# Kernel tuning notes

Measured on AMD Instinct MI355X. Metric: run time of the kernel, lower is better.

## Reference

```python
import jax, jax.numpy as jnp
import numpy as np

N_NODES = 40000

def setup_inputs() -> dict:
    key = jax.random.key(0)
    k1, k2, k3, k4 = jax.random.split(key, 4)
    x = jax.random.normal(k1, (N_NODES, 256), dtype=jnp.float32)
    edge_index = jax.random.randint(k2, (2, 640000), 0, N_NODES, dtype=jnp.int64)
    W = jax.random.normal(k3, (256, 128), dtype=jnp.float32) * (1.0 / np.sqrt(256))
    b = jax.random.normal(k4, (128,), dtype=jnp.float32) * 0.01
    return {"x": x, "edge_index": edge_index, "W": W, "b": b}

def reference(x, edge_index, W, b):
    N = x.shape[0]
    # GCNConv: add self-loops, symmetric degree normalization, linear, aggregate, bias
    loops = jnp.arange(N, dtype=edge_index.dtype)
    src = jnp.concatenate([edge_index[0], loops])  # message sources j
    dst = jnp.concatenate([edge_index[1], loops])  # targets i
    ones = jnp.ones_like(dst, dtype=x.dtype)
    deg = jax.ops.segment_sum(ones, dst, num_segments=N)  # in-degree incl. self-loop
    dinv = jnp.where(deg > 0, jax.lax.rsqrt(deg), 0.0)
    norm = dinv[src] * dinv[dst]  # [E+N]
    xw = x @ W  # transform first (in_dim -> out_dim), as in PyG GCNConv
    msgs = norm[:, None] * xw[src]  # [E+N, out_dim]
    agg = jax.ops.segment_sum(msgs, dst, num_segments=N) + b
    return jax.nn.relu(agg)  # dropout_value == 0 -> no dropout
```

## Files before the change

### kernel.cpp

```cpp
#include <hip/hip_runtime.h>

#define N_NODES 40000
#define IN_DIM 256
#define OUT_DIM 128
#define CAP 64
#define GEMM_BLOCKS 625
#define FILL_SLICES 160
#define FILL_RANGES 8
#define FILL_BLOCKS (FILL_SLICES * FILL_RANGES)
#define RANGE_SZ ((N_NODES + FILL_RANGES - 1) / FILL_RANGES)

typedef __bf16 bf16x8 __attribute__((ext_vector_type(8)));
typedef float floatx4 __attribute__((ext_vector_type(4)));

__device__ __forceinline__ int clamp_idx(int v) {
    unsigned u = (unsigned)v;
    return (u < (unsigned)N_NODES) ? v : 0;
}

__device__ __forceinline__ int get_idx(const void* p, long long i, int is64) {
    if (is64) return clamp_idx((int)((const long long*)p)[i]);
    return clamp_idx(((const int*)p)[i]);
}

__device__ __forceinline__ float bflo(unsigned u) {
    union { unsigned i; float f; } c; c.i = u << 16; return c.f;
}
__device__ __forceinline__ float bfhi(unsigned u) {
    union { unsigned i; float f; } c; c.i = u & 0xFFFF0000u; return c.f;
}

__global__ void prep_r13(const int* __restrict__ edge32, int* __restrict__ flag,
                         int* __restrict__ cnt, const float* __restrict__ W,
                         __bf16* __restrict__ wswz) {
    int i = blockIdx.x * 256 + threadIdx.x;
    if (i < N_NODES) cnt[i] = 0;
    if (i < IN_DIM * OUT_DIM) {
        int j    = i & 7;
        int lane = (i >> 3) & 63;
        int tile = i >> 9;
        int ct = tile & 7, kc = tile >> 3;
        int k = kc * 32 + (lane >> 4) * 8 + j;
        int n = ct * 16 + (lane & 15);
        wswz[i] = (__bf16)W[k * OUT_DIM + n];
    }
    if (blockIdx.x == 0) {
        __shared__ int sh[256];
        int t = threadIdx.x;
        int nz = 0;
        for (int k = t; k < 1000; k += 256) nz |= (edge32[2 * k + 1] != 0);
        sh[t] = nz;
        __syncthreads();
        for (int off = 128; off > 0; off >>= 1) {
            if (t < off) sh[t] |= sh[t + off];
            __syncthreads();
        }
        if (t == 0) *flag = sh[0] ? 0 : 1;
    }
}

__global__ __launch_bounds__(256) void main_r13(
    const float* __restrict__ x, const __bf16* __restrict__ wswz,
    __bf16* __restrict__ xwb,
    const void* __restrict__ edge, int E, const int* __restrict__ flag,
    int* __restrict__ cnt, unsigned short* __restrict__ bucket) {
    int t = threadIdx.x;
    if (blockIdx.x < GEMM_BLOCKS) {
        int wave = t >> 6, lane = t & 63;
        int quad = lane >> 4, m16 = lane & 15;
        int m = blockIdx.x * 64 + wave * 16 + m16;
        const float* xrow = x + (long long)m * IN_DIM;
        const bf16x8* wp = (const bf16x8*)wswz;

        floatx4 acc[8];
#pragma unroll
        for (int ct = 0; ct < 8; ++ct) acc[ct] = (floatx4){0.f, 0.f, 0.f, 0.f};

#pragma unroll
        for (int kc = 0; kc < 8; ++kc) {
            int k0 = kc * 32 + quad * 8;
            float4 xa = *(const float4*)(xrow + k0);
            float4 xb = *(const float4*)(xrow + k0 + 4);
            bf16x8 af;
            af[0] = (__bf16)xa.x; af[1] = (__bf16)xa.y;
            af[2] = (__bf16)xa.z; af[3] = (__bf16)xa.w;
            af[4] = (__bf16)xb.x; af[5] = (__bf16)xb.y;
            af[6] = (__bf16)xb.z; af[7] = (__bf16)xb.w;
#pragma unroll
            for (int ct = 0; ct < 8; ++ct) {
                bf16x8 bf = wp[(kc * 8 + ct) * 64 + lane];
                acc[ct] = __builtin_amdgcn_mfma_f32_16x16x32_bf16(af, bf, acc[ct], 0, 0, 0);
            }
        }

        int rbase = blockIdx.x * 64 + wave * 16 + quad * 4;
#pragma unroll
        for (int ct = 0; ct < 8; ++ct) {
            int col = ct * 16 + m16;
#pragma unroll
            for (int r = 0; r < 4; ++r)
                xwb[(long long)(rbase + r) * OUT_DIM + col] = (__bf16)acc[ct][r];
        }
    } else {
        int is64 = *flag;
        int fb = blockIdx.x - GEMM_BLOCKS;
        int range = blockIdx.x & 7;
        int slice = fb >> 3;
        int lo = range * RANGE_SZ;
        int slice_len = (E + FILL_SLICES - 1) / FILL_SLICES;
        int e0 = slice * slice_len;
        int e1 = e0 + slice_len; if (e1 > E) e1 = E;
        for (int e = e0 + t; e < e1; e += 256) {
            int d = get_idx(edge, (long long)E + e, is64);
            if ((unsigned)(d - lo) < (unsigned)RANGE_SZ) {
                int s = get_idx(edge, e, is64);
                int pos = atomicAdd(&cnt[d], 1);
                if (pos < CAP) bucket[d * CAP + pos] = (unsigned short)s;
            }
        }
    }
}

__global__ void gather_r13(const unsigned short* __restrict__ bucket,
                           const int* __restrict__ cnt,
                           const unsigned* __restrict__ xwd, const float* __restrict__ b,
                           float* __restrict__ out) {
    int node = blockIdx.x * 4 + (threadIdx.x >> 6);
    int lane = threadIdx.x & 63;
    if (node >= N_NODES) return;
    float b0 = b[2 * lane], b1 = b[2 * lane + 1];
    int cn_true = cnt[node];
    int take = cn_true < CAP ? cn_true : CAP;
    float dd = rsqrtf((float)(cn_true + 1));
    unsigned us = xwd[node * 64 + lane];
    float a0 = dd * dd * bflo(us);
    float a1 = dd * dd * bfhi(us);

    int s_l = 0; float nrm_l = 0.0f;
    if (lane < take) {
        s_l = (int)bucket[node * CAP + lane];
        nrm_l = dd * rsqrtf((float)(cnt[s_l] + 1));
    }
    int j = 0;
    for (; j + 8 <= take; j += 8) {
        int   s0 = __shfl(s_l, j),     s1 = __shfl(s_l, j + 1);
        int   s2 = __shfl(s_l, j + 2), s3 = __shfl(s_l, j + 3);
        int   s4 = __shfl(s_l, j + 4), s5 = __shfl(s_l, j + 5);
        int   s6 = __shfl(s_l, j + 6), s7 = __shfl(s_l, j + 7);
        float n0 = __shfl(nrm_l, j),     n1 = __shfl(nrm_l, j + 1);
        float n2 = __shfl(nrm_l, j + 2), n3 = __shfl(nrm_l, j + 3);
        float n4 = __shfl(nrm_l, j + 4), n5 = __shfl(nrm_l, j + 5);
        float n6 = __shfl(nrm_l, j + 6), n7 = __shfl(nrm_l, j + 7);
        unsigned u0 = xwd[s0 * 64 + lane], u1 = xwd[s1 * 64 + lane];
        unsigned u2 = xwd[s2 * 64 + lane], u3 = xwd[s3 * 64 + lane];
        unsigned u4 = xwd[s4 * 64 + lane], u5 = xwd[s5 * 64 + lane];
        unsigned u6 = xwd[s6 * 64 + lane], u7 = xwd[s7 * 64 + lane];
        a0 += n0 * bflo(u0); a1 += n0 * bfhi(u0);
        a0 += n1 * bflo(u1); a1 += n1 * bfhi(u1);
        a0 += n2 * bflo(u2); a1 += n2 * bfhi(u2);
        a0 += n3 * bflo(u3); a1 += n3 * bfhi(u3);
        a0 += n4 * bflo(u4); a1 += n4 * bfhi(u4);
        a0 += n5 * bflo(u5); a1 += n5 * bfhi(u5);
        a0 += n6 * bflo(u6); a1 += n6 * bfhi(u6);
        a0 += n7 * bflo(u7); a1 += n7 * bfhi(u7);
    }
    for (; j < take; ++j) {
        int   s = __shfl(s_l, j);
        float n = __shfl(nrm_l, j);
        unsigned u = xwd[s * 64 + lane];
        a0 += n * bflo(u); a1 += n * bfhi(u);
    }
    float2 r;
    r.x = fmaxf(a0 + b0, 0.0f);
    r.y = fmaxf(a1 + b1, 0.0f);
    *(float2*)&out[node * OUT_DIM + 2 * lane] = r;
}

extern "C" void kernel_launch(void* const* d_in, const int* in_sizes, int n_in,
                              void* d_out, int out_size, void* d_ws, size_t ws_size,
                              hipStream_t stream) {
    const float* x   = (const float*)d_in[0];
    const void* edge = d_in[1];
    const float* W   = (const float*)d_in[2];
    const float* b   = (const float*)d_in[3];
    float* out       = (float*)d_out;

    int E = in_sizes[1] / 2;

    char* ws = (char*)d_ws;
    int*            cnt    = (int*)(ws);
    int*            flag   = (int*)(ws + 160000);
    __bf16*         wswz   = (__bf16*)(ws + 160256);
    unsigned short* bucket = (unsigned short*)(ws + 225792);
    __bf16*         xwb    = (__bf16*)(ws + 5345792);

    prep_r13<<<160, 256, 0, stream>>>((const int*)edge, flag, cnt, W, wswz);
    main_r13<<<GEMM_BLOCKS + FILL_BLOCKS, 256, 0, stream>>>(
        x, wswz, xwb, edge, E, flag, cnt, bucket);
    gather_r13<<<N_NODES / 4, 256, 0, stream>>>(bucket, cnt, (const unsigned*)xwb, b, out);
}
```

Baseline: 157.7 us.

## Replace range-partitioned bucket fill with single-pass batched atomics; deepen gather unroll

The edge bucket fill no longer scans all edges eight times, once per destination range. Each thread now loads 8 consecutive edges, issues their atomics together, then writes the bucket entries, so the edge list is read once with more memory-level parallelism. Dropping range partitioning loses the destination locality of the atomics and bucket writes. The gather kernel also adds a 16-wide unrolled loop so more neighbor row loads are in flight, at the cost of more registers.

Result: no change. 154.8 us (-1.9%).

```diff
diff --git a/kernel.cpp b/kernel.cpp
--- a/kernel.cpp
+++ b/kernel.cpp
@@ -5,10 +5,8 @@
 #define OUT_DIM 128
 #define CAP 64
 #define GEMM_BLOCKS 625
-#define FILL_SLICES 160
-#define FILL_RANGES 8
-#define FILL_BLOCKS (FILL_SLICES * FILL_RANGES)
-#define RANGE_SZ ((N_NODES + FILL_RANGES - 1) / FILL_RANGES)
+#define EPT 8
+#define FILL_BLOCKS ((640000 + 256 * EPT - 1) / (256 * EPT))
 
 typedef __bf16 bf16x8 __attribute__((ext_vector_type(8)));
 typedef float floatx4 __attribute__((ext_vector_type(4)));
@@ -30,7 +28,7 @@
     union { unsigned i; float f; } c; c.i = u & 0xFFFF0000u; return c.f;
 }
 
-__global__ void prep_r13(const int* __restrict__ edge32, int* __restrict__ flag,
+__global__ void prep_r14(const int* __restrict__ edge32, int* __restrict__ flag,
                          int* __restrict__ cnt, const float* __restrict__ W,
                          __bf16* __restrict__ wswz) {
     int i = blockIdx.x * 256 + threadIdx.x;
@@ -59,7 +57,7 @@
     }
 }
 
-__global__ __launch_bounds__(256) void main_r13(
+__global__ __launch_bounds__(256) void main_r14(
     const float* __restrict__ x, const __bf16* __restrict__ wswz,
     __bf16* __restrict__ xwb,
     const void* __restrict__ edge, int E, const int* __restrict__ flag,
@@ -103,25 +101,24 @@
         }
     } else {
         int is64 = *flag;
-        int fb = blockIdx.x - GEMM_BLOCKS;
-        int range = blockIdx.x & 7;
-        int slice = fb >> 3;
-        int lo = range * RANGE_SZ;
-        int slice_len = (E + FILL_SLICES - 1) / FILL_SLICES;
-        int e0 = slice * slice_len;
-        int e1 = e0 + slice_len; if (e1 > E) e1 = E;
-        for (int e = e0 + t; e < e1; e += 256) {
-            int d = get_idx(edge, (long long)E + e, is64);
-            if ((unsigned)(d - lo) < (unsigned)RANGE_SZ) {
-                int s = get_idx(edge, e, is64);
-                int pos = atomicAdd(&cnt[d], 1);
-                if (pos < CAP) bucket[d * CAP + pos] = (unsigned short)s;
-            }
-        }
-    }
-}
-
-__global__ void gather_r13(const unsigned short* __restrict__ bucket,
+        int base = (blockIdx.x - GEMM_BLOCKS) * (256 * EPT) + t * EPT;
+        int s[EPT], d[EPT], p[EPT];
+#pragma unroll
+        for (int q = 0; q < EPT; ++q) {
+            int e = base + q;
+            s[q] = (e < E) ? get_idx(edge, e, is64) : 0;
+            d[q] = (e < E) ? get_idx(edge, (long long)E + e, is64) : 0;
+        }
+#pragma unroll
+        for (int q = 0; q < EPT; ++q)
+            p[q] = (base + q < E) ? atomicAdd(&cnt[d[q]], 1) : CAP;
+#pragma unroll
+        for (int q = 0; q < EPT; ++q)
+            if (p[q] < CAP) bucket[d[q] * CAP + p[q]] = (unsigned short)s[q];
+    }
+}
+
+__global__ void gather_r14(const unsigned short* __restrict__ bucket,
                            const int* __restrict__ cnt,
                            const unsigned* __restrict__ xwd, const float* __restrict__ b,
                            float* __restrict__ out) {
@@ -142,27 +139,33 @@
         nrm_l = dd * rsqrtf((float)(cnt[s_l] + 1));
     }
     int j = 0;
+    for (; j + 16 <= take; j += 16) {
+        unsigned uu[16]; float nn[16];
+#pragma unroll
+        for (int q = 0; q < 16; ++q) {
+            int s = __shfl(s_l, j + q);
+            nn[q] = __shfl(nrm_l, j + q);
+            uu[q] = xwd[s * 64 + lane];
+        }
+#pragma unroll
+        for (int q = 0; q < 16; ++q) {
+            a0 += nn[q] * bflo(uu[q]);
+            a1 += nn[q] * bfhi(uu[q]);
+        }
+    }
     for (; j + 8 <= take; j += 8) {
-        int   s0 = __shfl(s_l, j),     s1 = __shfl(s_l, j + 1);
-        int   s2 = __shfl(s_l, j + 2), s3 = __shfl(s_l, j + 3);
-        int   s4 = __shfl(s_l, j + 4), s5 = __shfl(s_l, j + 5);
-        int   s6 = __shfl(s_l, j + 6), s7 = __shfl(s_l, j + 7);
-        float n0 = __shfl(nrm_l, j),     n1 = __shfl(nrm_l, j + 1);
-        float n2 = __shfl(nrm_l, j + 2), n3 = __shfl(nrm_l, j + 3);
-        float n4 = __shfl(nrm_l, j + 4), n5 = __shfl(nrm_l, j + 5);
-        float n6 = __shfl(nrm_l, j + 6), n7 = __shfl(nrm_l, j + 7);
-        unsigned u0 = xwd[s0 * 64 + lane], u1 = xwd[s1 * 64 + lane];
-        unsigned u2 = xwd[s2 * 64 + lane], u3 = xwd[s3 * 64 + lane];
-        unsigned u4 = xwd[s4 * 64 + lane], u5 = xwd[s5 * 64 + lane];
-        unsigned u6 = xwd[s6 * 64 + lane], u7 = xwd[s7 * 64 + lane];
-        a0 += n0 * bflo(u0); a1 += n0 * bfhi(u0);
-        a0 += n1 * bflo(u1); a1 += n1 * bfhi(u1);
-        a0 += n2 * bflo(u2); a1 += n2 * bfhi(u2);
-        a0 += n3 * bflo(u3); a1 += n3 * bfhi(u3);
-        a0 += n4 * bflo(u4); a1 += n4 * bfhi(u4);
-        a0 += n5 * bflo(u5); a1 += n5 * bfhi(u5);
-        a0 += n6 * bflo(u6); a1 += n6 * bfhi(u6);
-        a0 += n7 * bflo(u7); a1 += n7 * bfhi(u7);
+        unsigned uu[8]; float nn[8];
+#pragma unroll
+        for (int q = 0; q < 8; ++q) {
+            int s = __shfl(s_l, j + q);
+            nn[q] = __shfl(nrm_l, j + q);
+            uu[q] = xwd[s * 64 + lane];
+        }
+#pragma unroll
+        for (int q = 0; q < 8; ++q) {
+            a0 += nn[q] * bflo(uu[q]);
+            a1 += nn[q] * bfhi(uu[q]);
+        }
     }
     for (; j < take; ++j) {
         int   s = __shfl(s_l, j);
@@ -194,8 +197,9 @@
     unsigned short* bucket = (unsigned short*)(ws + 225792);
     __bf16*         xwb    = (__bf16*)(ws + 5345792);
 
-    prep_r13<<<160, 256, 0, stream>>>((const int*)edge, flag, cnt, W, wswz);
-    main_r13<<<GEMM_BLOCKS + FILL_BLOCKS, 256, 0, stream>>>(
+    int fill_blocks = (E + 256 * EPT - 1) / (256 * EPT);
+    prep_r14<<<160, 256, 0, stream>>>((const int*)edge, flag, cnt, W, wswz);
+    main_r14<<<GEMM_BLOCKS + fill_blocks, 256, 0, stream>>>(
         x, wswz, xwb, edge, E, flag, cnt, bucket);
-    gather_r13<<<N_NODES / 4, 256, 0, stream>>>(bucket, cnt, (const unsigned*)xwb, b, out);
-}
+    gather_r14<<<N_NODES / 4, 256, 0, stream>>>(bucket, cnt, (const unsigned*)xwb, b, out);
+}
```
